# Optimization experiments

Hardware: AMD Instinct MI355X
Metric: run time of the kernel (lower is better)

## Reference

```python
import jax, jax.numpy as jnp
import numpy as np

NUM_V = 20000
N_EDGES = 160000
IN_CH, OUT_CH = 16, 32
IN_ORDER = OUT_ORDER = MID_ORDER = 2
N_RINGS = 2
BAND_LIMIT = 2
NUM_SAMPLES = 7


def build_kernel_basis(n_in, n_out, bl):
    """Equivariant kernel basis [num_bases, 2*bl+1, 2*n_out+1, 2*n_in+1].
    Freq axis layout: [const, cos(t), sin(t), cos(2t), sin(2t), ...] matching precomp."""
    Din, Dout, F = 2 * n_in + 1, 2 * n_out + 1, 2 * bl + 1
    I = np.eye(2)
    E = np.array([[0., -1.], [1., 0.]])   # rotation by pi/2
    S = np.array([[1., 0.], [0., -1.]])   # reflection
    ES = E @ S
    sl = lambda m: slice(0, 1) if m == 0 else slice(2 * m - 1, 2 * m + 1)
    bases = []

    def add(f, cos_blk, sin_blk, m, n):
        if f > bl:
            return
        B = np.zeros((F, Dout, Din))
        if f == 0:
            B[0, sl(m), sl(n)] = cos_blk
        else:
            B[2 * f - 1, sl(m), sl(n)] = cos_blk
            B[2 * f, sl(m), sl(n)] = sin_blk
        bases.append(B)

    for m in range(n_out + 1):
        for n in range(n_in + 1):
            if m == 0 and n == 0:
                add(0, np.ones((1, 1)), None, 0, 0)
            elif n == 0:  # scalar -> order-m pair: R(m t) e1, R(m t) e2
                add(m, np.array([[1.], [0.]]), np.array([[0.], [1.]]), m, 0)
                add(m, np.array([[0.], [1.]]), np.array([[-1.], [0.]]), m, 0)
            elif m == 0:  # order-n pair -> scalar: rows of R(-n t)
                add(n, np.array([[1., 0.]]), np.array([[0., 1.]]), 0, n)
                add(n, np.array([[0., 1.]]), np.array([[-1., 0.]]), 0, n)
            else:
                d = m - n
                f = abs(d)
                sg = 1.0 if d >= 0 else -1.0
                add(f, I, sg * E, m, n)          # R(d t)
                add(f, E, -sg * I, m, n)         # R(d t + pi/2)
                add(m + n, S, ES, m, n)          # R((m+n) t) S
                add(m + n, ES, -S, m, n)         # R((m+n) t + pi/2) S
    return np.stack(bases).astype(np.float32)


def fourier_mats(order, n):
    th = 2 * np.pi * np.arange(n) / n
    cols = [np.ones(n)]
    for m in range(1, order + 1):
        cols += [np.cos(m * th), np.sin(m * th)]
    T = np.stack(cols, 1)                              # [n_samples, 2*order+1]
    scale = np.array([1.0] + [2.0] * (2 * order)) / n
    Tinv = (T * scale).T                               # [2*order+1, n_samples]
    return jnp.asarray(T, jnp.float32), jnp.asarray(Tinv, jnp.float32)


def rep_act(x, alpha, order):
    """Gauge transport: rotate order-m feature pairs by m*alpha. x: [E,C,2*order+1]."""
    parts = [x[:, :, :1]]
    for m in range(1, order + 1):
        c = jnp.cos(m * alpha)[:, None]
        s = jnp.sin(m * alpha)[:, None]
        a, b = x[:, :, 2 * m - 1], x[:, :, 2 * m]
        parts.append(jnp.stack([c * a - s * b, s * a + c * b], axis=-1))
    return jnp.concatenate(parts, axis=-1)


def gem_conv(x, edge_index, precomp, connection, K, W, b, in_order):
    src, dst = edge_index[1], edge_index[0]
    xt = rep_act(x[src], connection, in_order)               # [E, Cin, Din] gather + transport
    wk = jnp.einsum('bfij,broc->froicj', K, W)               # fold basis with ring weights (small)
    t = jnp.einsum('ecj,froicj->efroi', xt, wk)              # per-edge freq/ring responses
    msg = jnp.einsum('efr,efroi->eoi', precomp, t)           # [E, Cout, Dout]
    out = jax.ops.segment_sum(msg, dst, num_segments=NUM_V)  # scatter-add to vertices
    return out.at[:, :, 0].add(b)                            # bias on scalar component


def regular_relu(x, order):
    T, Tinv = fourier_mats(order, NUM_SAMPLES)
    s = jnp.einsum('vcd,sd->vcs', x, T)   # irrep -> regular samples
    return jnp.einsum('vcs,ds->vcd', jax.nn.relu(s), Tinv)


def setup_inputs() -> dict:
    key = jax.random.key(0)
    k = jax.random.split(key, 8)
    nb = build_kernel_basis(IN_ORDER, MID_ORDER, BAND_LIMIT).shape[0]  # 19
    Din = 2 * IN_ORDER + 1
    x = jax.random.normal(k[0], (NUM_V, IN_CH, Din), jnp.float32)
    edge_index = jax.random.randint(k[1], (2, N_EDGES), 0, NUM_V, dtype=jnp.int32)
    precomp = jax.random.normal(k[2], (N_EDGES, 2 * BAND_LIMIT + 1, N_RINGS), jnp.float32)
    connection = jax.random.uniform(k[3], (N_EDGES,), jnp.float32) * (2 * np.pi)
    W1 = jax.random.normal(k[4], (nb, N_RINGS, OUT_CH, IN_CH), jnp.float32) * 0.1
    W2 = jax.random.normal(k[5], (nb, N_RINGS, OUT_CH, OUT_CH), jnp.float32) * 0.05
    W_lin = jax.random.normal(k[6], (OUT_CH, IN_CH), jnp.float32) * 0.1
    zeros = lambda: jnp.zeros((OUT_CH,), jnp.float32)
    return {"x": x, "edge_index": edge_index, "precomp": precomp, "connection": connection,
            "W1": W1, "b1": zeros(), "W2": W2, "b2": zeros(), "W_lin": W_lin, "b_lin": zeros()}


def reference(x, edge_index, precomp, connection, W1, b1, W2, b2, W_lin, b_lin):
    K = jnp.asarray(build_kernel_basis(IN_ORDER, MID_ORDER, BAND_LIMIT))  # orders equal -> shared basis
    y = gem_conv(x, edge_index, precomp, connection, K, W1, b1, IN_ORDER)
    y = regular_relu(y, MID_ORDER)
    y = gem_conv(y, edge_index, precomp, connection, K, W2, b2, MID_ORDER)
    res = jnp.einsum('vcd,oc->vod', x, W_lin) + b_lin[None, :, None]  # 1x1 conv residual
    o = min(y.shape[2], res.shape[2])
    y = y.at[:, :, :o].add(res[:, :, :o])
    return regular_relu(y, OUT_ORDER)
```

## Files before the change

kernel.cpp:

```cpp
#include <hip/hip_runtime.h>
#include <hip/hip_bf16.h>
#include <cstdint>

#define NV     20000
#define NE     160000
#define IC1    16
#define OC     32
#define DIN    5
#define NSLOT  49
#define NOUT   160
#define YSTR   165
struct SlotTables {
    int n;
    int b[64], f[64], i[64], j[64];
    float v[64];
};

constexpr SlotTables make_slots() {
    SlotTables T{};
    float K[19][5][5][5] = {};
    int nb = 0;
    const int BL = 2;
    auto add = [&](int f, const float (*cb)[2], const float (*sb)[2],
                   int m, int n) {
        if (f > BL) return;
        int r0 = (m == 0) ? 0 : (2 * m - 1), nr = (m == 0) ? 1 : 2;
        int c0 = (n == 0) ? 0 : (2 * n - 1), nc = (n == 0) ? 1 : 2;
        for (int a = 0; a < nr; a++)
            for (int bb = 0; bb < nc; bb++) {
                if (f == 0) {
                    K[nb][0][r0 + a][c0 + bb] = cb[a][bb];
                } else {
                    K[nb][2 * f - 1][r0 + a][c0 + bb] = cb[a][bb];
                    K[nb][2 * f    ][r0 + a][c0 + bb] = sb[a][bb];
                }
            }
        nb++;
    };
    const float ONE[2][2]  = {{1, 0}, {0, 0}};
    const float I2[2][2]   = {{1, 0}, {0, 1}};
    const float E2[2][2]   = {{0, -1}, {1, 0}};
    const float S2[2][2]   = {{1, 0}, {0, -1}};
    const float ES2[2][2]  = {{0, 1}, {1, 0}};
    const float NS2[2][2]  = {{-1, 0}, {0, 1}};
    const float C10[2][2]  = {{1, 0}, {0, 0}};
    const float C01[2][2]  = {{0, 0}, {1, 0}};
    const float CM10[2][2] = {{-1, 0}, {0, 0}};
    const float R10[2][2]  = {{1, 0}, {0, 0}};
    const float R01[2][2]  = {{0, 1}, {0, 0}};
    const float RM10[2][2] = {{-1, 0}, {0, 0}};

    for (int m = 0; m <= 2; m++)
        for (int n = 0; n <= 2; n++) {
            if (m == 0 && n == 0) {
                add(0, ONE, ONE, 0, 0);
            } else if (n == 0) {
                add(m, C10, C01, m, 0);
                add(m, C01, CM10, m, 0);
            } else if (m == 0) {
                add(n, R10, R01, 0, n);
                add(n, R01, RM10, 0, n);
            } else {
                int d = m - n;
                int f = d >= 0 ? d : -d;
                float sg = d >= 0 ? 1.f : -1.f;
                const float sgE[2][2]  = {{0, -sg}, {sg, 0}};
                const float msgI[2][2] = {{-sg, 0}, {0, -sg}};
                add(f, I2, sgE, m, n);
                add(f, E2, msgI, m, n);
                add(m + n, S2, ES2, m, n);
                add(m + n, ES2, NS2, m, n);
            }
        }
    T.n = 0;
    for (int i = 0; i < 5; i++)
        for (int b = 0; b < nb; b++)
            for (int f = 0; f < 5; f++)
                for (int j = 0; j < 5; j++)
                    if (K[b][f][i][j] != 0.0f) {
                        T.b[T.n] = b; T.f[T.n] = f; T.i[T.n] = i;
                        T.j[T.n] = j; T.v[T.n] = K[b][f][i][j];
                        T.n++;
                    }
    return T;
}

constexpr SlotTables SL = make_slots();
static_assert(SL.n == NSLOT, "expect 49 kernel-basis nonzeros");

__device__ __forceinline__ uint32_t bf16_rne(float f) {
    uint32_t u = __float_as_uint(f);
    u += 0x7fffu + ((u >> 16) & 1u);
    return u >> 16;
}

typedef __attribute__((ext_vector_type(8))) short bf16x8;
typedef __attribute__((ext_vector_type(4))) float f32x4;

template<int C>
__global__ __launch_bounds__(256) void build_M(const float* __restrict__ W,
                                               float* __restrict__ M) {
    int t = blockIdx.x * 256 + threadIdx.x;
    const int K = C * 50;
    if (t >= K * NOUT) return;
    int n = t % NOUT, k = t / NOUT;
    int o = n / 5, i = n % 5;
    int c = k / 50, r50 = k % 50;
    int j = r50 / 10, q = r50 % 10;
    int f = q >> 1, r = q & 1;
    float acc = 0.f;
    #pragma unroll
    for (int s = 0; s < NSLOT; s++) {
        if (SL.j[s] == j && SL.f[s] == f && SL.i[s] == i)
            acc += SL.v[s] * W[(size_t)((SL.b[s] * 2 + r) * 32 + o) * C + c];
    }
    M[(size_t)k * NOUT + n] = acc;
}

template<int K>
__global__ __launch_bounds__(256) void build_Mfrag(const float* __restrict__ M,
                                                   uint32_t* __restrict__ Mf) {
    int t = blockIdx.x * 256 + threadIdx.x;
    const int total = (K / 32) * 10 * 64 * 4;
    if (t >= total) return;
    int a = t & 3;
    int idx = t >> 2;
    int lane = idx & 63; idx >>= 6;
    int nt = idx % 10;
    int ck = idx / 10;
    int col = nt * 16 + (lane & 15);
    int k0 = ck * 32 + (lane >> 4) * 8 + 2 * a;
    uint32_t lo = bf16_rne(M[(size_t)k0 * NOUT + col]);
    uint32_t hi = bf16_rne(M[(size_t)(k0 + 1) * NOUT + col]);
    Mf[t] = lo | (hi << 16);
}

__global__ __launch_bounds__(256) void hist_k(const int* __restrict__ ei,
                                              int* __restrict__ counts) {
    int e = blockIdx.x * 256 + threadIdx.x;
    if (e < NE) atomicAdd(&counts[ei[e]], 1);
}

__global__ __launch_bounds__(1024) void scan_k(const int* __restrict__ counts,
                                               int* __restrict__ cursor) {
    __shared__ int part[1024];
    int t = threadIdx.x;
    int base = t * 20;
    int local[20];
    int s = 0;
    #pragma unroll
    for (int k = 0; k < 20; k++) {
        int idx = base + k;
        int c = (idx < NV) ? counts[idx] : 0;
        local[k] = c; s += c;
    }
    part[t] = s;
    __syncthreads();
    for (int off = 1; off < 1024; off <<= 1) {
        int add = (t >= off) ? part[t - off] : 0;
        __syncthreads();
        part[t] += add;
        __syncthreads();
    }
    int run = (t == 0) ? 0 : part[t - 1];
    #pragma unroll
    for (int k = 0; k < 20; k++) {
        int idx = base + k;
        if (idx < NV) { cursor[idx] = run; run += local[k]; }
    }
}

__global__ __launch_bounds__(256) void scatter_pack(const int* __restrict__ ei,
                                                    const float* __restrict__ pre,
                                                    const float* __restrict__ conn,
                                                    int* __restrict__ cursor,
                                                    int* __restrict__ SRC,
                                                    float4* __restrict__ REC) {
    int e = blockIdx.x * 256 + threadIdx.x;
    if (e == 0) {
        SRC[NE] = 0;
        REC[(size_t)NE * 3 + 0] = float4{0.f, 0.f, 0.f, 0.f};
        REC[(size_t)NE * 3 + 1] = float4{0.f, 0.f, 0.f, 0.f};
        REC[(size_t)NE * 3 + 2] = float4{0.f, 0.f, 0.f, 0.f};
    }
    if (e >= NE) return;
    int pos = atomicAdd(&cursor[ei[e]], 1);
    SRC[pos] = ei[NE + e];
    float al = conn[e];
    float c1 = __cosf(al), s1 = __sinf(al);
    const float* pp = pre + (size_t)e * 10;
    REC[(size_t)pos * 3 + 0] = float4{c1, s1, pp[0], pp[1]};
    REC[(size_t)pos * 3 + 1] = float4{pp[2], pp[3], pp[4], pp[5]};
    REC[(size_t)pos * 3 + 2] = float4{pp[6], pp[7], pp[8], pp[9]};
}

__global__ __launch_bounds__(256) void x_pack(const float* __restrict__ x,
                                              uint4* __restrict__ xb) {
    int t = blockIdx.x * 256 + threadIdx.x;
    if (t >= NV * IC1) return;
    const float* xr = x + (size_t)t * 5;
    uint4 o;
    o.x = bf16_rne(xr[0]) | (bf16_rne(xr[1]) << 16);
    o.y = bf16_rne(xr[2]) | (bf16_rne(xr[3]) << 16);
    o.z = bf16_rne(xr[4]);
    o.w = 0;
    xb[t] = o;
}

template<int C>
__global__ __launch_bounds__(256) void zbuild6(const uint4* __restrict__ xb,
                                               const int*   __restrict__ SRC,
                                               const float4* __restrict__ REC,
                                               const int* __restrict__ cursor,
                                               uint32_t* __restrict__ Z,
                                               int v0, int v1) {
    __shared__ uint32_t st[3200];
    int tid = threadIdx.x;
    int t = blockIdx.x * 256 + tid;
    int pair = t >> 1, h = t & 1;
    int npairs = (v1 - v0) * C;
    bool valid = pair < npairs;
    int c = pair % C;
    int v = v0 + (valid ? pair / C : 0);
    int beg = 0, end = 0;
    if (valid) { beg = (v == 0) ? 0 : cursor[v - 1]; end = cursor[v]; }

    float acc[25];
    #pragma unroll
    for (int z = 0; z < 25; z++) acc[z] = 0.f;

    int k = beg;
    if (k < end) {
        int k1 = (k + 1 < end) ? k + 1 : NE;
        int k2 = (k + 2 < end) ? k + 2 : NE;
        int s0 = SRC[k], s1i = SRC[k1], s2i = SRC[k2];
        const float4* rp = REC + (size_t)k * 3;
        float4 r0 = rp[0], r1 = rp[1], r2 = rp[2];
        uint4 u0 = xb[(size_t)s0 * C + c];
        uint4 u1 = xb[(size_t)s1i * C + c];
        while (true) {
            bool more = (k1 != NE);
            int k3 = (k + 3 < end) ? k + 3 : NE;
            int s3i = SRC[k3];
            uint4 u2 = xb[(size_t)s2i * C + c];
            const float4* rpn = REC + (size_t)k1 * 3;
            float4 n0 = rpn[0], n1 = rpn[1], n2 = rpn[2];
            float x0 = __uint_as_float(u0.x << 16);
            float x1 = __uint_as_float(u0.x & 0xffff0000u);
            float x2 = __uint_as_float(u0.y << 16);
            float x3 = __uint_as_float(u0.y & 0xffff0000u);
            float x4 = __uint_as_float(u0.z << 16);
            float cc1 = r0.x, ss1 = r0.y;
            float cc2 = cc1 * cc1 - ss1 * ss1, ss2 = 2.f * cc1 * ss1;
            float xt[5];
            xt[0] = x0;
            xt[1] = cc1 * x1 - ss1 * x2;
            xt[2] = ss1 * x1 + cc1 * x2;
            xt[3] = cc2 * x3 - ss2 * x4;
            xt[4] = ss2 * x3 + cc2 * x4;
            float ph[5];
            ph[0] = h ? r1.w : r0.z;
            ph[1] = h ? r2.x : r0.w;
            ph[2] = h ? r2.y : r1.x;
            ph[3] = h ? r2.z : r1.y;
            ph[4] = h ? r2.w : r1.z;
            #pragma unroll
            for (int j = 0; j < 5; j++)
                #pragma unroll
                for (int w = 0; w < 5; w++)
                    acc[j * 5 + w] = fmaf(xt[j], ph[w], acc[j * 5 + w]);
            if (!more) break;
            k = k1; k1 = k2; k2 = k3;
            r0 = n0; r1 = n1; r2 = n2;
            u0 = u1; u1 = u2;
            s2i = s3i;
        }
    }
    uint32_t* sb = st + (tid >> 1) * 25;
    #pragma unroll
    for (int j = 0; j < 5; j++) {
        float q5v = __shfl_xor(acc[j * 5 + 0], 1);
        if (h == 0) {
            sb[j * 5 + 0] = bf16_rne(acc[j * 5 + 0]) | (bf16_rne(acc[j * 5 + 1]) << 16);
            sb[j * 5 + 1] = bf16_rne(acc[j * 5 + 2]) | (bf16_rne(acc[j * 5 + 3]) << 16);
            sb[j * 5 + 2] = bf16_rne(acc[j * 5 + 4]) | (bf16_rne(q5v) << 16);
        } else {
            sb[j * 5 + 3] = bf16_rne(acc[j * 5 + 1]) | (bf16_rne(acc[j * 5 + 2]) << 16);
            sb[j * 5 + 4] = bf16_rne(acc[j * 5 + 3]) | (bf16_rne(acc[j * 5 + 4]) << 16);
        }
    }
    __syncthreads();
    size_t gbase = (size_t)blockIdx.x * 3200;
    int pbase = blockIdx.x * 128;
    for (int i = tid; i < 3200; i += 256)
        if (pbase + i / 25 < npairs) Z[gbase + i] = st[i];
}

__device__ __forceinline__ void fourier_relu(float d0, float d1, float d2,
                                             float d3, float d4, float* out5) {
    float o0 = 0, o1 = 0, o2 = 0, o3 = 0, o4 = 0;
    #pragma unroll
    for (int k = 0; k < 7; k++) {
        float th = (float)k * (6.28318530717958647692f / 7.0f);
        float ck = __cosf(th), sk = __sinf(th);
        float c2k = ck * ck - sk * sk, s2k = 2.f * ck * sk;
        float sv = d0 + ck * d1 + sk * d2 + c2k * d3 + s2k * d4;
        sv = fmaxf(sv, 0.f);
        o0 += sv; o1 += sv * ck; o2 += sv * sk; o3 += sv * c2k; o4 += sv * s2k;
    }
    const float i7 = 1.0f / 7.0f;
    out5[0] = o0 * i7; out5[1] = o1 * (2.f * i7); out5[2] = o2 * (2.f * i7);
    out5[3] = o3 * (2.f * i7); out5[4] = o4 * (2.f * i7);
}

template<int K, int EPI>
__global__ __launch_bounds__(256) void gemm_fused(const uint32_t* __restrict__ Z,
                                                  const uint32_t* __restrict__ Mf,
                                                  int rows,
                                                  uint4* __restrict__ y1b,
                                                  const float* __restrict__ bias,
                                                  const float* __restrict__ xres,
                                                  const float* __restrict__ Wl,
                                                  const float* __restrict__ bl,
                                                  float* __restrict__ outp) {
    constexpr int NC = K / 32;
    __shared__ uint4 Bs[2][640];
    __shared__ float Ys[64 * YSTR];
    int t = threadIdx.x;
    int lane = t & 63;
    int wave = t >> 6;
    int r0 = blockIdx.x * 64 + wave * 16;
    int mrow = lane & 15;
    int q = lane >> 4;
    int ra = r0 + mrow;
    if (ra >= rows) ra = rows - 1;
    const uint32_t* za = Z + (size_t)ra * (K / 2) + q * 4;
    const uint4* mfg = (const uint4*)Mf + lane;

    auto stage = [&](int ck, int nb) {
        const uint4* gp = mfg + (size_t)ck * 640;
        for (int i = wave; i < 10; i += 4)
            __builtin_amdgcn_global_load_lds(
                (const __attribute__((address_space(1))) void*)(gp + i * 64),
                (__attribute__((address_space(3))) void*)(&Bs[nb][i * 64]),
                16, 0, 0);
    };

    f32x4 acc[10];
    #pragma unroll
    for (int nt = 0; nt < 10; nt++) acc[nt] = {0.f, 0.f, 0.f, 0.f};

    stage(0, 0);
    bf16x8 af = *(const bf16x8*)za;
    __syncthreads();

    for (int ck = 0; ck < NC; ck++) {
        int buf = ck & 1;
        bf16x8 af_n = af;
        if (ck + 1 < NC) {
            stage(ck + 1, buf ^ 1);
            af_n = *(const bf16x8*)(za + (ck + 1) * 16);
        }
        bf16x8 bf[10];
        #pragma unroll
        for (int nt = 0; nt < 10; nt++)
            bf[nt] = *(const bf16x8*)&Bs[buf][nt * 64 + lane];
        #pragma unroll
        for (int nt = 0; nt < 10; nt++)
            acc[nt] = __builtin_amdgcn_mfma_f32_16x16x32_bf16(af, bf[nt],
                                                              acc[nt], 0, 0, 0);
        af = af_n;
        __syncthreads();
    }
    #pragma unroll
    for (int nt = 0; nt < 10; nt++) {
        int col = nt * 16 + mrow;
        #pragma unroll
        for (int reg = 0; reg < 4; reg++) {
            int r = wave * 16 + q * 4 + reg;
            Ys[r * YSTR + col] = acc[nt][reg];
        }
    }
    __syncthreads();
    #pragma unroll
    for (int it = 0; it < 8; it++) {
        int item = t + it * 256;
        int row = item >> 5, ch = item & 31;
        int vr = blockIdx.x * 64 + row;
        if (vr >= rows) continue;
        const float* yr = &Ys[row * YSTR + ch * 5];
        float d0 = yr[0], d1 = yr[1], d2 = yr[2], d3 = yr[3], d4 = yr[4];
        float r5[5];
        if (EPI == 1) {
            d0 += bias[ch];
            fourier_relu(d0, d1, d2, d3, d4, r5);
            uint4 o;
            o.x = bf16_rne(r5[0]) | (bf16_rne(r5[1]) << 16);
            o.y = bf16_rne(r5[2]) | (bf16_rne(r5[3]) << 16);
            o.z = bf16_rne(r5[4]);
            o.w = 0;
            y1b[(size_t)vr * 32 + ch] = o;
        } else {
            float rr0 = 0, rr1 = 0, rr2 = 0, rr3 = 0, rr4 = 0;
            const float* xb = xres + (size_t)vr * (IC1 * DIN);
            const float* wl = Wl + ch * IC1;
            #pragma unroll
            for (int c = 0; c < IC1; c++) {
                float w = wl[c];
                rr0 = fmaf(w, xb[c * 5 + 0], rr0);
                rr1 = fmaf(w, xb[c * 5 + 1], rr1);
                rr2 = fmaf(w, xb[c * 5 + 2], rr2);
                rr3 = fmaf(w, xb[c * 5 + 3], rr3);
                rr4 = fmaf(w, xb[c * 5 + 4], rr4);
            }
            float blo = bl[ch];
            d0 += bias[ch] + rr0 + blo;
            d1 += rr1 + blo;
            d2 += rr2 + blo;
            d3 += rr3 + blo;
            d4 += rr4 + blo;
            fourier_relu(d0, d1, d2, d3, d4, r5);
            float* ob = outp + ((size_t)vr * 32 + ch) * 5;
            #pragma unroll
            for (int d = 0; d < 5; d++) ob[d] = r5[d];
        }
    }
}

extern "C" void kernel_launch(void* const* d_in, const int* in_sizes, int n_in,
                              void* d_out, int out_size, void* d_ws, size_t ws_size,
                              hipStream_t stream) {
    const float* x    = (const float*)d_in[0];
    const int*   ei   = (const int*)  d_in[1];
    const float* pre  = (const float*)d_in[2];
    const float* conn = (const float*)d_in[3];
    const float* W1   = (const float*)d_in[4];
    const float* b1   = (const float*)d_in[5];
    const float* W2   = (const float*)d_in[6];
    const float* b2   = (const float*)d_in[7];
    const float* Wl   = (const float*)d_in[8];
    const float* bl   = (const float*)d_in[9];
    float* out = (float*)d_out;

    const int K1 = IC1 * 50;
    const int K2 = OC  * 50;

    const size_t Y_BYTES   = (size_t)NV * NOUT * sizeof(float);
    const size_t M1_BYTES  = (size_t)K1 * NOUT * sizeof(float);
    const size_t M2_BYTES  = (size_t)K2 * NOUT * sizeof(float);
    const size_t MF1_BYTES = (size_t)(K1 / 32) * 10 * 64 * 16;
    const size_t MF2_BYTES = (size_t)(K2 / 32) * 10 * 64 * 16;
    const size_t CSR_BYTES = (size_t)(2 * NV) * sizeof(int);
    const size_t REC_BYTES = (size_t)(NE + 1) * 48;
    const size_t SRC_BYTES = (((size_t)(NE + 1) * 4 + 15) / 16) * 16;
    const size_t Y1B_BYTES = (size_t)NV * OC * 16;
    char* ws = (char*)d_ws;
    float* M1 = (float*)(ws);
    float* M2 = (float*)(ws + M1_BYTES);
    uint32_t* Mf1 = (uint32_t*)(ws + M1_BYTES + M2_BYTES);
    uint32_t* Mf2 = (uint32_t*)(ws + M1_BYTES + M2_BYTES + MF1_BYTES);
    int* counts = (int*)(ws + M1_BYTES + M2_BYTES + MF1_BYTES + MF2_BYTES);
    int* cursor = counts + NV;
    size_t csr_end = M1_BYTES + M2_BYTES + MF1_BYTES + MF2_BYTES + CSR_BYTES;
    float4* REC = (float4*)(ws + csr_end);
    int*    SRC = (int*)(ws + csr_end + REC_BYTES);
    uint4*  Y1B = (uint4*)(ws + csr_end + REC_BYTES + SRC_BYTES);
    uint4*  XB1 = Y1B;
    size_t fixed = csr_end + REC_BYTES + SRC_BYTES + Y1B_BYTES;

    size_t tail = (ws_size > fixed) ? (ws_size - fixed) : 0;
    uint32_t* zbuf;
    size_t zcap;
    if (tail >= Y_BYTES) { zbuf = (uint32_t*)(ws + fixed); zcap = tail; }
    else                 { zbuf = (uint32_t*)d_out;        zcap = Y_BYTES; }
    int chunk1 = (int)(zcap / ((size_t)K1 * 2)); if (chunk1 > NV) chunk1 = NV;
    int chunk2 = (int)(zcap / ((size_t)K2 * 2)); if (chunk2 > NV) chunk2 = NV;

    hipMemsetAsync(counts, 0, NV * sizeof(int), stream);

    build_M<IC1><<<(K1 * NOUT + 255) / 256, 256, 0, stream>>>(W1, M1);
    build_M<OC> <<<(K2 * NOUT + 255) / 256, 256, 0, stream>>>(W2, M2);
    build_Mfrag<K1><<<((K1 / 32) * 2560 + 255) / 256, 256, 0, stream>>>(M1, Mf1);
    build_Mfrag<K2><<<((K2 / 32) * 2560 + 255) / 256, 256, 0, stream>>>(M2, Mf2);

    hist_k<<<(NE + 255) / 256, 256, 0, stream>>>(ei, counts);
    scan_k<<<1, 1024, 0, stream>>>(counts, cursor);
    scatter_pack<<<(NE + 255) / 256, 256, 0, stream>>>(ei, pre, conn, cursor,
                                                       SRC, REC);
    x_pack<<<(NV * IC1 + 255) / 256, 256, 0, stream>>>(x, XB1);

    for (int v0 = 0; v0 < NV; v0 += chunk1) {
        int v1 = v0 + chunk1; if (v1 > NV) v1 = NV;
        int rows = v1 - v0;
        zbuild6<IC1><<<((size_t)rows * IC1 * 2 + 255) / 256, 256, 0, stream>>>(
            XB1, SRC, REC, cursor, zbuf, v0, v1);
        gemm_fused<K1, 1><<<(rows + 63) / 64, 256, 0, stream>>>(
            zbuf, Mf1, rows, Y1B + (size_t)v0 * 32, b1,
            nullptr, nullptr, nullptr, nullptr);
    }
    for (int v0 = 0; v0 < NV; v0 += chunk2) {
        int v1 = v0 + chunk2; if (v1 > NV) v1 = NV;
        int rows = v1 - v0;
        zbuild6<OC><<<((size_t)rows * OC * 2 + 255) / 256, 256, 0, stream>>>(
            Y1B, SRC, REC, cursor, zbuf, v0, v1);
        gemm_fused<K2, 2><<<(rows + 63) / 64, 256, 0, stream>>>(
            zbuf, Mf2, rows, nullptr, b2,
            x + (size_t)v0 * (IC1 * DIN), Wl, bl, out + (size_t)v0 * NOUT);
    }
}
```

Before: 274.6 us.

## Split GEMM K-loop across waves, load B fragments directly, stage residual in LDS

The fused GEMM now gives each block 32 rows and splits the K reduction across two wave pairs, which combine partial sums through shared memory. B fragments are loaded straight from global memory into registers with software prefetch instead of being double-buffered through LDS with a barrier per chunk. The residual x rows are staged in LDS for the second-layer epilogue, and chunk sizes are evened out across launches. This gives twice as many blocks and fewer barriers, at the cost of redundant global B reads per wave and an extra LDS reduction pass.

```diff
diff --git a/kernel.cpp b/kernel.cpp
--- a/kernel.cpp
+++ b/kernel.cpp
@@ -324,69 +324,85 @@
                                                   const float* __restrict__ bl,
                                                   float* __restrict__ outp) {
     constexpr int NC = K / 32;
-    __shared__ uint4 Bs[2][640];
-    __shared__ float Ys[64 * YSTR];
+    constexpr int NCH0 = (NC + 1) / 2;
+    __shared__ float Ys[32 * YSTR];
+    __shared__ float Xs[EPI == 2 ? 32 * 80 : 1];
     int t = threadIdx.x;
     int lane = t & 63;
     int wave = t >> 6;
-    int r0 = blockIdx.x * 64 + wave * 16;
+    int rowg = wave & 1, kh = wave >> 1;
+    int r0 = blockIdx.x * 32 + rowg * 16;
     int mrow = lane & 15;
     int q = lane >> 4;
     int ra = r0 + mrow;
     if (ra >= rows) ra = rows - 1;
     const uint32_t* za = Z + (size_t)ra * (K / 2) + q * 4;
-    const uint4* mfg = (const uint4*)Mf + lane;
-
-    auto stage = [&](int ck, int nb) {
-        const uint4* gp = mfg + (size_t)ck * 640;
-        for (int i = wave; i < 10; i += 4)
-            __builtin_amdgcn_global_load_lds(
-                (const __attribute__((address_space(1))) void*)(gp + i * 64),
-                (__attribute__((address_space(3))) void*)(&Bs[nb][i * 64]),
-                16, 0, 0);
-    };
+    const bf16x8* mfg = (const bf16x8*)((const uint4*)Mf + lane);
+
+    int cka = kh ? NCH0 : 0;
+    int ckz = kh ? NC : NCH0;
 
     f32x4 acc[10];
     #pragma unroll
     for (int nt = 0; nt < 10; nt++) acc[nt] = {0.f, 0.f, 0.f, 0.f};
 
-    stage(0, 0);
-    bf16x8 af = *(const bf16x8*)za;
-    __syncthreads();
-
-    for (int ck = 0; ck < NC; ck++) {
-        int buf = ck & 1;
-        bf16x8 af_n = af;
-        if (ck + 1 < NC) {
-            stage(ck + 1, buf ^ 1);
-            af_n = *(const bf16x8*)(za + (ck + 1) * 16);
-        }
-        bf16x8 bf[10];
+    bf16x8 af = *(const bf16x8*)(za + (size_t)cka * 16);
+    bf16x8 bfr[10];
+    #pragma unroll
+    for (int nt = 0; nt < 10; nt++)
+        bfr[nt] = mfg[((size_t)cka * 10 + nt) * 64];
+
+    for (int ck = cka; ck < ckz; ck++) {
+        bf16x8 afn = af;
+        bf16x8 bfn[10];
+        #pragma unroll
+        for (int nt = 0; nt < 10; nt++) bfn[nt] = bfr[nt];
+        if (ck + 1 < ckz) {
+            afn = *(const bf16x8*)(za + (size_t)(ck + 1) * 16);
+            #pragma unroll
+            for (int nt = 0; nt < 10; nt++)
+                bfn[nt] = mfg[((size_t)(ck + 1) * 10 + nt) * 64];
+        }
         #pragma unroll
         for (int nt = 0; nt < 10; nt++)
-            bf[nt] = *(const bf16x8*)&Bs[buf][nt * 64 + lane];
+            acc[nt] = __builtin_amdgcn_mfma_f32_16x16x32_bf16(af, bfr[nt],
+                                                              acc[nt], 0, 0, 0);
+        af = afn;
         #pragma unroll
-        for (int nt = 0; nt < 10; nt++)
-            acc[nt] = __builtin_amdgcn_mfma_f32_16x16x32_bf16(af, bf[nt],
-                                                              acc[nt], 0, 0, 0);
-        af = af_n;
-        __syncthreads();
-    }
-    #pragma unroll
-    for (int nt = 0; nt < 10; nt++) {
-        int col = nt * 16 + mrow;
+        for (int nt = 0; nt < 10; nt++) bfr[nt] = bfn[nt];
+    }
+
+    if (EPI == 2) {
+        int gbase = blockIdx.x * 32 * 80;
+        int glim = rows * 80;
+        for (int i = t; i < 32 * 80; i += 256)
+            Xs[i] = (gbase + i < glim) ? xres[gbase + i] : 0.f;
+    }
+    if (kh == 0) {
         #pragma unroll
-        for (int reg = 0; reg < 4; reg++) {
-            int r = wave * 16 + q * 4 + reg;
-            Ys[r * YSTR + col] = acc[nt][reg];
+        for (int nt = 0; nt < 10; nt++) {
+            int col = nt * 16 + mrow;
+            #pragma unroll
+            for (int reg = 0; reg < 4; reg++)
+                Ys[(rowg * 16 + q * 4 + reg) * YSTR + col] = acc[nt][reg];
         }
     }
     __syncthreads();
-    #pragma unroll
-    for (int it = 0; it < 8; it++) {
+    if (kh == 1) {
+        #pragma unroll
+        for (int nt = 0; nt < 10; nt++) {
+            int col = nt * 16 + mrow;
+            #pragma unroll
+            for (int reg = 0; reg < 4; reg++)
+                Ys[(rowg * 16 + q * 4 + reg) * YSTR + col] += acc[nt][reg];
+        }
+    }
+    __syncthreads();
+    #pragma unroll
+    for (int it = 0; it < 4; it++) {
         int item = t + it * 256;
         int row = item >> 5, ch = item & 31;
-        int vr = blockIdx.x * 64 + row;
+        int vr = blockIdx.x * 32 + row;
         if (vr >= rows) continue;
         const float* yr = &Ys[row * YSTR + ch * 5];
         float d0 = yr[0], d1 = yr[1], d2 = yr[2], d3 = yr[3], d4 = yr[4];
@@ -402,16 +418,16 @@
             y1b[(size_t)vr * 32 + ch] = o;
         } else {
             float rr0 = 0, rr1 = 0, rr2 = 0, rr3 = 0, rr4 = 0;
-            const float* xb = xres + (size_t)vr * (IC1 * DIN);
+            const float* xs = &Xs[row * 80];
             const float* wl = Wl + ch * IC1;
             #pragma unroll
             for (int c = 0; c < IC1; c++) {
                 float w = wl[c];
-                rr0 = fmaf(w, xb[c * 5 + 0], rr0);
-                rr1 = fmaf(w, xb[c * 5 + 1], rr1);
-                rr2 = fmaf(w, xb[c * 5 + 2], rr2);
-                rr3 = fmaf(w, xb[c * 5 + 3], rr3);
-                rr4 = fmaf(w, xb[c * 5 + 4], rr4);
+                rr0 = fmaf(w, xs[c * 5 + 0], rr0);
+                rr1 = fmaf(w, xs[c * 5 + 1], rr1);
+                rr2 = fmaf(w, xs[c * 5 + 2], rr2);
+                rr3 = fmaf(w, xs[c * 5 + 3], rr3);
+                rr4 = fmaf(w, xs[c * 5 + 4], rr4);
             }
             float blo = bl[ch];
             d0 += bias[ch] + rr0 + blo;
@@ -475,6 +491,8 @@
     else                 { zbuf = (uint32_t*)d_out;        zcap = Y_BYTES; }
     int chunk1 = (int)(zcap / ((size_t)K1 * 2)); if (chunk1 > NV) chunk1 = NV;
     int chunk2 = (int)(zcap / ((size_t)K2 * 2)); if (chunk2 > NV) chunk2 = NV;
+    int nch1 = (NV + chunk1 - 1) / chunk1; chunk1 = (NV + nch1 - 1) / nch1;
+    int nch2 = (NV + chunk2 - 1) / chunk2; chunk2 = (NV + nch2 - 1) / nch2;
 
     hipMemsetAsync(counts, 0, NV * sizeof(int), stream);
 
@@ -494,7 +512,7 @@
         int rows = v1 - v0;
         zbuild6<IC1><<<((size_t)rows * IC1 * 2 + 255) / 256, 256, 0, stream>>>(
             XB1, SRC, REC, cursor, zbuf, v0, v1);
-        gemm_fused<K1, 1><<<(rows + 63) / 64, 256, 0, stream>>>(
+        gemm_fused<K1, 1><<<(rows + 31) / 32, 256, 0, stream>>>(
             zbuf, Mf1, rows, Y1B + (size_t)v0 * 32, b1,
             nullptr, nullptr, nullptr, nullptr);
     }
@@ -503,7 +521,7 @@
         int rows = v1 - v0;
         zbuild6<OC><<<((size_t)rows * OC * 2 + 255) / 256, 256, 0, stream>>>(
             Y1B, SRC, REC, cursor, zbuf, v0, v1);
-        gemm_fused<K2, 2><<<(rows + 63) / 64, 256, 0, stream>>>(
+        gemm_fused<K2, 2><<<(rows + 31) / 32, 256, 0, stream>>>(
             zbuf, Mf2, rows, nullptr, b2,
             x + (size_t)v0 * (IC1 * DIN), Wl, bl, out + (size_t)v0 * NOUT);
     }
```

New measurement: 267.0 us. 1.03x faster.
